# Performance work log

Hardware: AMD Instinct MI355X
Metric: run time of the kernel (lower is better)

Reference implementation:

```python
import math
import jax, jax.numpy as jnp
import numpy as np

D_MODEL = 1024
HID = 128
H, NB = 16, 16


def setup_inputs() -> dict:
    key = jax.random.key(0)
    ks = jax.random.split(key, 8)
    B, L = 4, 4096
    theta_path = jax.random.normal(ks[0], (B, L, H, NB), dtype=jnp.float32)
    content_emb = jax.random.normal(ks[1], (B, L, D_MODEL), dtype=jnp.float32)
    # measure_head params (PyTorch Linear default init: U(-1/sqrt(fan_in), 1/sqrt(fan_in)))
    s1 = 1.0 / math.sqrt(D_MODEL)
    s2 = 1.0 / math.sqrt(HID)
    W1 = jax.random.uniform(ks[2], (D_MODEL, HID), minval=-s1, maxval=s1, dtype=jnp.float32)
    b1 = jax.random.uniform(ks[3], (HID,), minval=-s1, maxval=s1, dtype=jnp.float32)
    W2 = jax.random.uniform(ks[4], (HID, H * NB), minval=-s2, maxval=s2, dtype=jnp.float32)
    b2 = jax.random.uniform(ks[5], (H * NB,), minval=-s2, maxval=s2, dtype=jnp.float32)
    log_Pi = jnp.zeros((H, NB), dtype=jnp.float32)
    log_R = jnp.zeros((H, NB), dtype=jnp.float32)
    return {"theta_path": theta_path, "content_emb": content_emb, "W1": W1, "b1": b1,
            "W2": W2, "b2": b2, "log_Pi": log_Pi, "log_R": log_R}


def _affine_scan(alpha, u):
    # d_t = alpha_t * d_{t-1} + u_t, d_0 = u_0 (zero initial state), scan over axis=1 (L)
    def combine(left, right):
        a_l, u_l = left
        a_r, u_r = right
        return a_l * a_r, a_r * u_l + u_r
    _, d = jax.lax.associative_scan(combine, (alpha, u), axis=1)
    return d


def reference(theta_path, content_emb, W1, b1, W2, b2, log_Pi, log_R):
    B, L, _, _ = theta_path.shape
    h = jax.nn.gelu(content_emb @ W1 + b1, approximate=False)  # [B,L,128], exact GELU as torch
    z = jnp.pi * jnp.tanh((h @ W2 + b2).reshape(B, L, H, NB))
    diff = z - theta_path
    nu = jnp.arctan2(jnp.sin(diff), jnp.cos(diff))  # wrapped angle residual
    Pi = jnp.exp(log_Pi)[None, None]  # [1,1,H,NB]
    R = jnp.exp(log_R)[None, None]
    K = Pi / jnp.maximum(Pi + R, 1e-08)
    Kf = jnp.broadcast_to(K, (B, L, H, NB))
    alpha = 1.0 - Kf
    u = Kf * nu
    d = _affine_scan(alpha, u)
    return (theta_path + d,
            jnp.broadcast_to(Pi, (B, L, H, NB)),
            Kf,
            jnp.broadcast_to(R, (B, L, H, NB)))
```

## Files before the change

### kernel.cpp

```cpp
#include <hip/hip_runtime.h>
#include <math.h>

#define MTOT  16384
#define DM    1024
#define HIDN  128
#define HNB   256
#define NBAT  4
#define CLK   32
#define NBLK  512
#define CPB   128

typedef _Float16 v8h __attribute__((ext_vector_type(8)));
typedef float    v4f __attribute__((ext_vector_type(4)));
#define MFMA16(a,b,c) __builtin_amdgcn_mfma_f32_16x16x32_f16((a),(b),(c),0,0,0)

#define W1TILE  16384
#define W2BASE  524288
#define W2TILE  32768
#define BLOB_BYTES 655360

#define RAWOFF 0
#define AHOFF  16384
#define ALOFF  20480
#define W1OFF  24576
#define HHOFF  40960
#define HLOFF  49664
#define ZOFF   0
#define SMEMSZ 73728

#define VMCNT_(N) asm volatile("s_waitcnt vmcnt(" #N ")" ::: "memory")
#define VMCNT(N) VMCNT_(N)
#define BARRIER() do { asm volatile("s_waitcnt lgkmcnt(0)" ::: "memory"); \
                       __builtin_amdgcn_s_barrier(); } while (0)

typedef const __attribute__((address_space(1))) void* gas1_t;
typedef __attribute__((address_space(3))) void* las3_t;

__device__ __forceinline__ void gld16(const void* g, void* l) {
    __builtin_amdgcn_global_load_lds((gas1_t)g, (las3_t)l, 16, 0, 0);
}

__global__ __launch_bounds__(256) void k_prep(
    const float* __restrict__ W1,
    const float* __restrict__ W2,
    char* __restrict__ blobs)
{
    __shared__ float lds[32][260];
    const int t = threadIdx.x, blk = blockIdx.x;
    if (blk < 32) {
        const int k0 = blk * 32;
        #pragma unroll
        for (int i = 0; i < 4; ++i) {
            int j = t + i * 256;
            int k = j >> 5, n4 = (j & 31) << 2;
            *(float4*)&lds[k][n4] = *(const float4*)&W1[(size_t)(k0 + k) * HIDN + n4];
        }
        __syncthreads();
        const int n = t >> 1, kh = t & 1;
        #pragma unroll
        for (int si = 0; si < 2; ++si) {
            const int s = 2 * kh + si;
            union { _Float16 h[8]; int4 v; } H, L;
            #pragma unroll
            for (int e = 0; e < 8; ++e) {
                float v = lds[s * 8 + e][n];
                _Float16 hh = (_Float16)v;
                H.h[e] = hh;
                L.h[e] = (_Float16)((v - (float)hh) * 4096.f);
            }
            char* d = blobs + blk * W1TILE + n * 64 + ((s ^ (n & 3)) << 4);
            *(int4*)d = H.v;
            *(int4*)(d + 8192) = L.v;
        }
    } else {
        const int ks = blk - 32, k0 = ks * 32;
        #pragma unroll
        for (int i = 0; i < 8; ++i) {
            int j = t + i * 256;
            int k = j >> 6, n4 = (j & 63) << 2;
            *(float4*)&lds[k][n4] = *(const float4*)&W2[(size_t)(k0 + k) * HNB + n4];
        }
        __syncthreads();
        const int n = t;
        #pragma unroll
        for (int s = 0; s < 4; ++s) {
            union { _Float16 h[8]; int4 v; } H, L;
            #pragma unroll
            for (int e = 0; e < 8; ++e) {
                float v = lds[s * 8 + e][n];
                _Float16 hh = (_Float16)v;
                H.h[e] = hh;
                L.h[e] = (_Float16)((v - (float)hh) * 4096.f);
            }
            char* d = blobs + W2BASE + ks * W2TILE + n * 64 + ((s ^ (n & 3)) << 4);
            *(int4*)d = H.v;
            *(int4*)(d + 16384) = L.v;
        }
    }
}

__global__ __launch_bounds__(512, 4) void k_mega(
    const float* __restrict__ A,
    const float* __restrict__ theta,
    const float* __restrict__ b1, const float* __restrict__ b2,
    const float* __restrict__ logPi, const float* __restrict__ logR,
    const char* __restrict__ blobs,
    float* __restrict__ out0, float* __restrict__ out2,
    float* fill1, float* fill3,
    float* carry, int cstride)
{
    __shared__ __attribute__((aligned(16))) char smem[SMEMSZ];

    const int tid  = threadIdx.x;
    const int blk  = blockIdx.x;
    const int m0   = blk * CLK;
    const int lane = tid & 63;
    const int wid  = tid >> 6;
    const int ln15 = lane & 15;
    const int q    = lane >> 4;
    const int np   = wid & 3;
    const int mh   = wid >> 2;

    const int rrow = (wid & 3) * 8 + (lane >> 3);
    const float* aStage = A + (size_t)(m0 + rrow) * DM + (lane & 7) * 4;
    const int rawDst = rrow * 128 + (lane & 7) * 16;

    const int crow = (wid & 3) * 8 + (lane >> 3);
    const int cvtRd = crow * 128 + (lane & 7) * 16;
    const int cs = (lane & 7) >> 1, chalf = (lane & 7) & 1;
    const int cvtWr = crow * 64 + ((cs ^ ((crow >> 1) & 3)) << 4) + chalf * 8;

    const int wq = wid & 3;
    const char* wSrcB = blobs + wq * 4096 + lane * 16;
    const int   wDstB = wq * 4096 + lane * 16;

    const int arow = 16 * mh + ln15;
    const int aby  = arow * 64 + ((q ^ ((arow >> 1) & 3)) << 4);
    const int col0 = 32 * np + ln15;
    const int col1 = col0 + 16;
    const int wo0  = col0 * 64 + ((q ^ (col0 & 3)) << 4);
    const int wo1  = col1 * 64 + ((q ^ (col1 & 3)) << 4);

    v4f acc1[2], acc2[2];
    acc1[0] = acc1[1] = (v4f){0.f, 0.f, 0.f, 0.f};
    acc2[0] = acc2[1] = (v4f){0.f, 0.f, 0.f, 0.f};

#define CVT(J) do { \
    const char* rb_ = smem + ((J) % 4) * 4096 + cvtRd; \
    v4f rv_ = *(const v4f*)rb_; \
    union { _Float16 h[4]; int2 i; } H_, L_; \
    _Pragma("unroll") \
    for (int e_ = 0; e_ < 4; ++e_) { \
        _Float16 t_ = (_Float16)rv_[e_]; \
        H_.h[e_] = t_; \
        L_.h[e_] = (_Float16)((rv_[e_] - (float)t_) * 4096.f); \
    } \
    *(int2*)(smem + AHOFF + ((J) & 1) * 2048 + cvtWr) = H_.i; \
    *(int2*)(smem + ALOFF + ((J) & 1) * 2048 + cvtWr) = L_.i; \
} while (0)

#define STEP(KT, RVM, WVM, DO_RAW, DO_W, DO_CVT) do { \
    if (wid < 4) { \
        if (DO_RAW) gld16(aStage + (size_t)((KT) + 4) * 32, \
                          smem + ((KT) % 4) * 4096 + rawDst); \
    } else if (DO_W) { \
        const char* ws_ = wSrcB + (size_t)((KT) + 2) * W1TILE; \
        char* wd_ = smem + W1OFF + (((KT) + 2) % 3) * W1TILE + wDstB; \
        gld16(ws_, wd_);                 gld16(ws_ + 1024, wd_ + 1024); \
        gld16(ws_ + 2048, wd_ + 2048);   gld16(ws_ + 3072, wd_ + 3072); \
    } \
    { \
        const char* abH = smem + AHOFF + ((KT) & 1) * 2048; \
        const char* abL = smem + ALOFF + ((KT) & 1) * 2048; \
        const char* wbB = smem + W1OFF + ((KT) % 3) * W1TILE; \
        v8h ah_  = *(const v8h*)(abH + aby); \
        v8h al_  = *(const v8h*)(abL + aby); \
        v8h wh0_ = *(const v8h*)(wbB + wo0); \
        v8h wl0_ = *(const v8h*)(wbB + 8192 + wo0); \
        v8h wh1_ = *(const v8h*)(wbB + wo1); \
        v8h wl1_ = *(const v8h*)(wbB + 8192 + wo1); \
        acc1[0] = MFMA16(ah_, wh0_, acc1[0]); \
        acc2[0] = MFMA16(ah_, wl0_, acc2[0]); \
        acc2[0] = MFMA16(al_, wh0_, acc2[0]); \
        acc1[1] = MFMA16(ah_, wh1_, acc1[1]); \
        acc2[1] = MFMA16(ah_, wl1_, acc2[1]); \
        acc2[1] = MFMA16(al_, wh1_, acc2[1]); \
    } \
    if (wid < 4) { VMCNT(RVM); if (DO_CVT) { CVT((KT) + 1); } } \
    else         { VMCNT(WVM); } \
    BARRIER(); \
} while (0)

    if (wid < 4) {
        gld16(aStage,      smem + 0 * 4096 + rawDst);
        gld16(aStage + 32, smem + 1 * 4096 + rawDst);
        gld16(aStage + 64, smem + 2 * 4096 + rawDst);
        gld16(aStage + 96, smem + 3 * 4096 + rawDst);
        VMCNT(3);
        CVT(0);
    } else {
        #pragma unroll
        for (int t = 0; t < 3; ++t) {
            const char* ws_ = wSrcB + (size_t)t * W1TILE;
            char* wd_ = smem + W1OFF + t * W1TILE + wDstB;
            gld16(ws_, wd_);               gld16(ws_ + 1024, wd_ + 1024);
            gld16(ws_ + 2048, wd_ + 2048); gld16(ws_ + 3072, wd_ + 3072);
        }
        VMCNT(8);
    }
    BARRIER();

    STEP(0,3,4,1,1,1);  STEP(1,3,4,1,1,1);  STEP(2,3,4,1,1,1);  STEP(3,3,4,1,1,1);
    STEP(4,3,4,1,1,1);  STEP(5,3,4,1,1,1);  STEP(6,3,4,1,1,1);  STEP(7,3,4,1,1,1);
    STEP(8,3,4,1,1,1);  STEP(9,3,4,1,1,1);  STEP(10,3,4,1,1,1); STEP(11,3,4,1,1,1);
    STEP(12,3,4,1,1,1); STEP(13,3,4,1,1,1); STEP(14,3,4,1,1,1); STEP(15,3,4,1,1,1);
    STEP(16,3,4,1,1,1); STEP(17,3,4,1,1,1); STEP(18,3,4,1,1,1); STEP(19,3,4,1,1,1);
    STEP(20,3,4,1,1,1); STEP(21,3,4,1,1,1); STEP(22,3,4,1,1,1); STEP(23,3,4,1,1,1);
    STEP(24,3,4,1,1,1); STEP(25,3,4,1,1,1); STEP(26,3,4,1,1,1); STEP(27,3,4,1,1,1);
    STEP(28,2,4,0,1,1); STEP(29,1,4,0,1,1); STEP(30,0,0,0,0,1); STEP(31,0,0,0,0,0);

    const float inv = 1.f / 4096.f;
    #pragma unroll
    for (int ni = 0; ni < 2; ++ni) {
        const int col = 32 * np + 16 * ni + ln15;
        const float bv = b1[col];
        #pragma unroll
        for (int r = 0; r < 4; ++r) {
            const int row = 16 * mh + 4 * q + r;
            float y = acc1[ni][r] + acc2[ni][r] * inv + bv;
            float h = 0.5f * y * (1.f + erff(y * 0.70710678118654752f));
            _Float16 hh = (_Float16)h;
            _Float16 hl = (_Float16)((h - (float)hh) * 4096.f);
            const int byte_ = row * 272 + ((((col >> 3) ^ ((row >> 1) & 3))) << 4)
                            + (col & 7) * 2;
            *(_Float16*)(smem + HHOFF + byte_) = hh;
            *(_Float16*)(smem + HLOFF + byte_) = hl;
        }
    }
    BARRIER();

    v4f c1[4], c2[4];
    #pragma unroll
    for (int i = 0; i < 4; ++i) {
        c1[i] = (v4f){0.f, 0.f, 0.f, 0.f};
        c2[i] = (v4f){0.f, 0.f, 0.f, 0.f};
    }
    const int hrow = 16 * mh + ln15;
    #pragma unroll
    for (int ks = 0; ks < 4; ++ks) {
        const int hby = hrow * 272 + ((4 * ks + (q ^ ((hrow >> 1) & 3))) << 4);
        v8h hh = *(const v8h*)(smem + HHOFF + hby);
        v8h hl = *(const v8h*)(smem + HLOFF + hby);
        v8h w2h[4], w2l[4];
        #pragma unroll
        for (int ni = 0; ni < 4; ++ni) {
            const int c2i = 64 * np + 16 * ni + ln15;
            const char* wp = blobs + W2BASE + (size_t)ks * W2TILE
                           + c2i * 64 + ((q ^ (c2i & 3)) << 4);
            w2h[ni] = *(const v8h*)(wp);
            w2l[ni] = *(const v8h*)(wp + 16384);
        }
        #pragma unroll
        for (int ni = 0; ni < 4; ++ni) {
            c1[ni] = MFMA16(hh, w2h[ni], c1[ni]);
            c2[ni] = MFMA16(hh, w2l[ni], c2[ni]);
            c2[ni] = MFMA16(hl, w2h[ni], c2[ni]);
        }
    }

    #pragma unroll
    for (int ni = 0; ni < 4; ++ni) {
        const int col = 64 * np + 16 * ni + ln15;
        const float bv = b2[col];
        #pragma unroll
        for (int r = 0; r < 4; ++r) {
            const int row = 16 * mh + 4 * q + r;
            float y2 = c1[ni][r] + c2[ni][r] * inv + bv;
            *(float*)(smem + ZOFF + row * 1040 + col * 4) =
                3.14159265358979323846f * tanhf(y2);
        }
    }
    BARRIER();

    if (tid < 256) {
        const int c = tid;
        const float Pi = expf(logPi[c]);
        const float Rr = expf(logR[c]);
        const float Kc = Pi / fmaxf(Pi + Rr, 1e-8f);
        const float alpha = 1.f - Kc;
        float d = 0.f;
        float tv[2][16];
        #pragma unroll
        for (int i = 0; i < 16; ++i)
            tv[0][i] = theta[(size_t)(m0 + i) * HNB + c];
        #pragma unroll
        for (int g = 0; g < 2; ++g) {
            if (g < 1) {
                #pragma unroll
                for (int i = 0; i < 16; ++i)
                    tv[1][i] = theta[(size_t)(m0 + 16 + i) * HNB + c];
            }
            float sv[16];
            #pragma unroll
            for (int i = 0; i < 16; ++i) {
                float z = *(const float*)(smem + ZOFF + (g * 16 + i) * 1040 + c * 4);
                float diff = z - tv[g][i];
                float kq = rintf(diff * 0.15915494309189533577f);
                float nu = (float)((double)diff - (double)kq * 6.283185307179586476925286766559);
                d = fmaf(alpha, d, Kc * nu);
                sv[i] = tv[g][i] + d;
            }
            #pragma unroll
            for (int i = 0; i < 16; ++i)
                out0[(size_t)(m0 + g * 16 + i) * HNB + c] = sv[i];
        }
        carry[(size_t)blk * cstride + c] = d;
    } else {
        const int c = tid - 256;
        const float Pi = expf(logPi[c]);
        const float Rr = expf(logR[c]);
        const float Kc = Pi / fmaxf(Pi + Rr, 1e-8f);
        if (fill1) {
            #pragma unroll 4
            for (int i = 0; i < CLK; ++i) {
                size_t idx = (size_t)(m0 + i) * HNB + c;
                out2[idx]  = Kc;
                fill1[idx] = Pi;
                fill3[idx] = Rr;
            }
        } else {
            #pragma unroll 4
            for (int i = 0; i < CLK; ++i)
                out2[(size_t)(m0 + i) * HNB + c] = Kc;
        }
    }
#undef STEP
#undef CVT
}

__global__ __launch_bounds__(256) void k_cscan(
    const float* __restrict__ logPi, const float* __restrict__ logR,
    float* carry, int cstride)
{
    const int c = threadIdx.x, b = blockIdx.x;
    const float Pi = expf(logPi[c]);
    const float Rr = expf(logR[c]);
    const float alpha = 1.f - Pi / fmaxf(Pi + Rr, 1e-8f);
    float A32 = alpha;
    #pragma unroll
    for (int i = 0; i < 5; ++i) A32 *= A32;
    float D = 0.f;
    for (int s0 = 0; s0 < CPB; s0 += 16) {
        float a[16];
        #pragma unroll
        for (int j = 0; j < 16; ++j)
            a[j] = carry[(size_t)(b * CPB + s0 + j) * cstride + c];
        #pragma unroll
        for (int j = 0; j < 16; ++j) {
            carry[(size_t)(b * CPB + s0 + j) * cstride + c] = D;
            D = fmaf(A32, D, a[j]);
        }
    }
}

__global__ __launch_bounds__(256) void k_apply(
    const float* __restrict__ logPi, const float* __restrict__ logR,
    float* __restrict__ out0, float* out1, float* out3,
    const float* carry, int cstride, int do_fills)
{
    const int blk = blockIdx.x;
    const int c = threadIdx.x;
    const float Pi = expf(logPi[c]);
    const float Rr = expf(logR[c]);
    const float Kc = Pi / fmaxf(Pi + Rr, 1e-8f);
    const float alpha = 1.f - Kc;
    float D = carry[(size_t)blk * cstride + c];
    float w = alpha * D;
    const size_t base = (size_t)blk * (CLK * HNB) + c;
    if (do_fills) {
        #pragma unroll 4
        for (int i = 0; i < CLK; ++i) {
            size_t idx = base + (size_t)i * HNB;
            out0[idx] += w;
            out1[idx] = Pi;
            out3[idx] = Rr;
            w *= alpha;
        }
    } else {
        #pragma unroll 4
        for (int i = 0; i < CLK; ++i) {
            size_t idx = base + (size_t)i * HNB;
            out0[idx] += w;
            w *= alpha;
        }
    }
}

extern "C" void kernel_launch(void* const* d_in, const int* in_sizes, int n_in,
                              void* d_out, int out_size, void* d_ws, size_t ws_size,
                              hipStream_t stream) {
    const float* theta   = (const float*)d_in[0];
    const float* content = (const float*)d_in[1];
    const float* W1      = (const float*)d_in[2];
    const float* b1      = (const float*)d_in[3];
    const float* W2      = (const float*)d_in[4];
    const float* b2      = (const float*)d_in[5];
    const float* logPi   = (const float*)d_in[6];
    const float* logR    = (const float*)d_in[7];

    float* out  = (float*)d_out;
    float* out0 = out;
    float* out1 = out + (size_t)MTOT * HNB;
    float* out2 = out + (size_t)2 * MTOT * HNB;
    float* out3 = out + (size_t)3 * MTOT * HNB;

    const size_t carry_bytes = (size_t)NBLK * 256 * 4;
    const size_t need = carry_bytes + BLOB_BYTES;
    float* carry; int cstride, do_fills; char* blobs;
    float *f1, *f3;
    if (ws_size >= need) {
        carry   = (float*)d_ws;
        cstride = 256;
        blobs   = (char*)d_ws + carry_bytes;
        f1 = out1; f3 = out3; do_fills = 0;
    } else {
        carry   = out3;
        cstride = CLK * HNB;
        blobs   = (char*)out1;
        f1 = nullptr; f3 = nullptr; do_fills = 1;
    }

    hipLaunchKernelGGL(k_prep, dim3(36), dim3(256), 0, stream, W1, W2, blobs);
    hipLaunchKernelGGL(k_mega, dim3(NBLK), dim3(512), 0, stream,
                       content, theta, b1, b2, logPi, logR, blobs,
                       out0, out2, f1, f3, carry, cstride);
    hipLaunchKernelGGL(k_cscan, dim3(NBAT), dim3(256), 0, stream,
                       logPi, logR, carry, cstride);
    hipLaunchKernelGGL(k_apply, dim3(NBLK), dim3(256), 0, stream,
                       logPi, logR, out0, out1, out3, carry, cstride, do_fills);
}
```

Measured before the change: 62.00 us.

## Store weights in MFMA fragment order and convert A in registers

Repacks the W1 and W2 half-precision split blobs into per-lane MFMA fragment order, so each lane loads one contiguous 16-byte chunk and the XOR swizzle is no longer needed. The A tile is loaded raw into LDS already in fragment order, and each wave now does the fp32 to hi/lo fp16 split in registers just before its MFMAs. This drops the separate CVT stage, its double-buffered converted-A LDS region, and the extra LDS write/read round trip. LDS usage drops to 64KB and the A prefetch depth goes from 4 tiles to 3, which may shorten latency hiding while improving occupancy headroom.

```diff
diff --git a/kernel.cpp b/kernel.cpp
--- a/kernel.cpp
+++ b/kernel.cpp
@@ -20,13 +20,11 @@
 #define BLOB_BYTES 655360
 
 #define RAWOFF 0
-#define AHOFF  16384
-#define ALOFF  20480
-#define W1OFF  24576
-#define HHOFF  40960
-#define HLOFF  49664
-#define ZOFF   0
-#define SMEMSZ 73728
+#define W1OFF  16384
+#define HHOFF  0
+#define HLOFF  8192
+#define ZOFF   16384
+#define SMEMSZ 65536
 
 #define VMCNT_(N) asm volatile("s_waitcnt vmcnt(" #N ")" ::: "memory")
 #define VMCNT(N) VMCNT_(N)
@@ -56,19 +54,20 @@
             *(float4*)&lds[k][n4] = *(const float4*)&W1[(size_t)(k0 + k) * HIDN + n4];
         }
         __syncthreads();
-        const int n = t >> 1, kh = t & 1;
-        #pragma unroll
-        for (int si = 0; si < 2; ++si) {
-            const int s = 2 * kh + si;
+        const int fl = t & 63, np = t >> 6;
+        const int kb = (fl >> 4) * 8;
+        #pragma unroll
+        for (int fi = 0; fi < 2; ++fi) {
+            const int col = 32 * np + 16 * fi + (fl & 15);
             union { _Float16 h[8]; int4 v; } H, L;
             #pragma unroll
             for (int e = 0; e < 8; ++e) {
-                float v = lds[s * 8 + e][n];
+                float v = lds[kb + e][col];
                 _Float16 hh = (_Float16)v;
                 H.h[e] = hh;
                 L.h[e] = (_Float16)((v - (float)hh) * 4096.f);
             }
-            char* d = blobs + blk * W1TILE + n * 64 + ((s ^ (n & 3)) << 4);
+            char* d = blobs + blk * W1TILE + np * 2048 + fi * 1024 + fl * 16;
             *(int4*)d = H.v;
             *(int4*)(d + 8192) = L.v;
         }
@@ -81,18 +80,21 @@
             *(float4*)&lds[k][n4] = *(const float4*)&W2[(size_t)(k0 + k) * HNB + n4];
         }
         __syncthreads();
-        const int n = t;
-        #pragma unroll
-        for (int s = 0; s < 4; ++s) {
+        const int fl = t & 63, cg0 = t >> 6;
+        const int kb = (fl >> 4) * 8;
+        #pragma unroll
+        for (int i = 0; i < 4; ++i) {
+            const int cg = cg0 * 4 + i;
+            const int col = cg * 16 + (fl & 15);
             union { _Float16 h[8]; int4 v; } H, L;
             #pragma unroll
             for (int e = 0; e < 8; ++e) {
-                float v = lds[s * 8 + e][n];
+                float v = lds[kb + e][col];
                 _Float16 hh = (_Float16)v;
                 H.h[e] = hh;
                 L.h[e] = (_Float16)((v - (float)hh) * 4096.f);
             }
-            char* d = blobs + W2BASE + ks * W2TILE + n * 64 + ((s ^ (n & 3)) << 4);
+            char* d = blobs + W2BASE + ks * W2TILE + cg * 1024 + fl * 16;
             *(int4*)d = H.v;
             *(int4*)(d + 16384) = L.v;
         }
@@ -121,118 +123,99 @@
     const int np   = wid & 3;
     const int mh   = wid >> 2;
 
-    const int rrow = (wid & 3) * 8 + (lane >> 3);
-    const float* aStage = A + (size_t)(m0 + rrow) * DM + (lane & 7) * 4;
-    const int rawDst = rrow * 128 + (lane & 7) * 16;
-
-    const int crow = (wid & 3) * 8 + (lane >> 3);
-    const int cvtRd = crow * 128 + (lane & 7) * 16;
-    const int cs = (lane & 7) >> 1, chalf = (lane & 7) & 1;
-    const int cvtWr = crow * 64 + ((cs ^ ((crow >> 1) & 3)) << 4) + chalf * 8;
+    const int mh_s = wid >> 1, half_s = wid & 1;
+    const float* aSrc = A + (size_t)(m0 + 16 * mh_s + ln15) * DM + q * 8 + half_s * 4;
+    const int rawDst = wid * 1024 + lane * 16;
 
     const int wq = wid & 3;
-    const char* wSrcB = blobs + wq * 4096 + lane * 16;
-    const int   wDstB = wq * 4096 + lane * 16;
-
-    const int arow = 16 * mh + ln15;
-    const int aby  = arow * 64 + ((q ^ ((arow >> 1) & 3)) << 4);
-    const int col0 = 32 * np + ln15;
-    const int col1 = col0 + 16;
-    const int wo0  = col0 * 64 + ((q ^ (col0 & 3)) << 4);
-    const int wo1  = col1 * 64 + ((q ^ (col1 & 3)) << 4);
+    const char* wSrc = blobs + wq * 2048 + (size_t)lane * 16;
+    const int   wDst = wq * 2048 + lane * 16;
 
     v4f acc1[2], acc2[2];
     acc1[0] = acc1[1] = (v4f){0.f, 0.f, 0.f, 0.f};
     acc2[0] = acc2[1] = (v4f){0.f, 0.f, 0.f, 0.f};
 
-#define CVT(J) do { \
-    const char* rb_ = smem + ((J) % 4) * 4096 + cvtRd; \
-    v4f rv_ = *(const v4f*)rb_; \
-    union { _Float16 h[4]; int2 i; } H_, L_; \
-    _Pragma("unroll") \
-    for (int e_ = 0; e_ < 4; ++e_) { \
-        _Float16 t_ = (_Float16)rv_[e_]; \
-        H_.h[e_] = t_; \
-        L_.h[e_] = (_Float16)((rv_[e_] - (float)t_) * 4096.f); \
-    } \
-    *(int2*)(smem + AHOFF + ((J) & 1) * 2048 + cvtWr) = H_.i; \
-    *(int2*)(smem + ALOFF + ((J) & 1) * 2048 + cvtWr) = L_.i; \
-} while (0)
-
-#define STEP(KT, RVM, WVM, DO_RAW, DO_W, DO_CVT) do { \
+#define STEP(KT, AV, WV, DO_RAW, DO_W) do { \
     if (wid < 4) { \
-        if (DO_RAW) gld16(aStage + (size_t)((KT) + 4) * 32, \
-                          smem + ((KT) % 4) * 4096 + rawDst); \
+        if (DO_RAW) gld16(aSrc + (size_t)((KT) + 3) * 32, \
+                          smem + RAWOFF + (((KT) + 3) & 3) * 4096 + rawDst); \
     } else if (DO_W) { \
-        const char* ws_ = wSrcB + (size_t)((KT) + 2) * W1TILE; \
-        char* wd_ = smem + W1OFF + (((KT) + 2) % 3) * W1TILE + wDstB; \
-        gld16(ws_, wd_);                 gld16(ws_ + 1024, wd_ + 1024); \
-        gld16(ws_ + 2048, wd_ + 2048);   gld16(ws_ + 3072, wd_ + 3072); \
+        const char* ws_ = wSrc + (size_t)((KT) + 2) * W1TILE; \
+        char* wd_ = smem + W1OFF + (((KT) + 2) % 3) * 16384 + wDst; \
+        gld16(ws_, wd_);             gld16(ws_ + 1024, wd_ + 1024); \
+        gld16(ws_ + 8192, wd_ + 8192); gld16(ws_ + 9216, wd_ + 9216); \
     } \
     { \
-        const char* abH = smem + AHOFF + ((KT) & 1) * 2048; \
-        const char* abL = smem + ALOFF + ((KT) & 1) * 2048; \
-        const char* wbB = smem + W1OFF + ((KT) % 3) * W1TILE; \
-        v8h ah_  = *(const v8h*)(abH + aby); \
-        v8h al_  = *(const v8h*)(abL + aby); \
-        v8h wh0_ = *(const v8h*)(wbB + wo0); \
-        v8h wl0_ = *(const v8h*)(wbB + 8192 + wo0); \
-        v8h wh1_ = *(const v8h*)(wbB + wo1); \
-        v8h wl1_ = *(const v8h*)(wbB + 8192 + wo1); \
-        acc1[0] = MFMA16(ah_, wh0_, acc1[0]); \
-        acc2[0] = MFMA16(ah_, wl0_, acc2[0]); \
-        acc2[0] = MFMA16(al_, wh0_, acc2[0]); \
-        acc1[1] = MFMA16(ah_, wh1_, acc1[1]); \
-        acc2[1] = MFMA16(ah_, wl1_, acc2[1]); \
-        acc2[1] = MFMA16(al_, wh1_, acc2[1]); \
+        const char* rawb = smem + RAWOFF + ((KT) & 3) * 4096 + mh * 2048 + lane * 16; \
+        v4f lo = *(const v4f*)rawb; \
+        v4f hi = *(const v4f*)(rawb + 1024); \
+        const char* wbB = smem + W1OFF + ((KT) % 3) * 16384 + np * 2048 + lane * 16; \
+        v8h wh0 = *(const v8h*)(wbB); \
+        v8h wh1 = *(const v8h*)(wbB + 1024); \
+        v8h wl0 = *(const v8h*)(wbB + 8192); \
+        v8h wl1 = *(const v8h*)(wbB + 9216); \
+        v8h ah, al; \
+        _Pragma("unroll") \
+        for (int e_ = 0; e_ < 4; ++e_) { \
+            _Float16 t0_ = (_Float16)lo[e_]; \
+            ah[e_] = t0_; \
+            al[e_] = (_Float16)((lo[e_] - (float)t0_) * 4096.f); \
+            _Float16 t1_ = (_Float16)hi[e_]; \
+            ah[e_ + 4] = t1_; \
+            al[e_ + 4] = (_Float16)((hi[e_] - (float)t1_) * 4096.f); \
+        } \
+        acc1[0] = MFMA16(ah, wh0, acc1[0]); \
+        acc2[0] = MFMA16(ah, wl0, acc2[0]); \
+        acc2[0] = MFMA16(al, wh0, acc2[0]); \
+        acc1[1] = MFMA16(ah, wh1, acc1[1]); \
+        acc2[1] = MFMA16(ah, wl1, acc2[1]); \
+        acc2[1] = MFMA16(al, wh1, acc2[1]); \
     } \
-    if (wid < 4) { VMCNT(RVM); if (DO_CVT) { CVT((KT) + 1); } } \
-    else         { VMCNT(WVM); } \
+    if (wid < 4) { VMCNT(AV); } else { VMCNT(WV); } \
     BARRIER(); \
 } while (0)
 
     if (wid < 4) {
-        gld16(aStage,      smem + 0 * 4096 + rawDst);
-        gld16(aStage + 32, smem + 1 * 4096 + rawDst);
-        gld16(aStage + 64, smem + 2 * 4096 + rawDst);
-        gld16(aStage + 96, smem + 3 * 4096 + rawDst);
-        VMCNT(3);
-        CVT(0);
+        gld16(aSrc,      smem + RAWOFF + 0 * 4096 + rawDst);
+        gld16(aSrc + 32, smem + RAWOFF + 1 * 4096 + rawDst);
+        gld16(aSrc + 64, smem + RAWOFF + 2 * 4096 + rawDst);
+        VMCNT(2);
     } else {
         #pragma unroll
-        for (int t = 0; t < 3; ++t) {
-            const char* ws_ = wSrcB + (size_t)t * W1TILE;
-            char* wd_ = smem + W1OFF + t * W1TILE + wDstB;
+        for (int t2 = 0; t2 < 2; ++t2) {
+            const char* ws_ = wSrc + (size_t)t2 * W1TILE;
+            char* wd_ = smem + W1OFF + t2 * 16384 + wDst;
             gld16(ws_, wd_);               gld16(ws_ + 1024, wd_ + 1024);
-            gld16(ws_ + 2048, wd_ + 2048); gld16(ws_ + 3072, wd_ + 3072);
-        }
-        VMCNT(8);
+            gld16(ws_ + 8192, wd_ + 8192); gld16(ws_ + 9216, wd_ + 9216);
+        }
+        VMCNT(4);
     }
     BARRIER();
 
-    STEP(0,3,4,1,1,1);  STEP(1,3,4,1,1,1);  STEP(2,3,4,1,1,1);  STEP(3,3,4,1,1,1);
-    STEP(4,3,4,1,1,1);  STEP(5,3,4,1,1,1);  STEP(6,3,4,1,1,1);  STEP(7,3,4,1,1,1);
-    STEP(8,3,4,1,1,1);  STEP(9,3,4,1,1,1);  STEP(10,3,4,1,1,1); STEP(11,3,4,1,1,1);
-    STEP(12,3,4,1,1,1); STEP(13,3,4,1,1,1); STEP(14,3,4,1,1,1); STEP(15,3,4,1,1,1);
-    STEP(16,3,4,1,1,1); STEP(17,3,4,1,1,1); STEP(18,3,4,1,1,1); STEP(19,3,4,1,1,1);
-    STEP(20,3,4,1,1,1); STEP(21,3,4,1,1,1); STEP(22,3,4,1,1,1); STEP(23,3,4,1,1,1);
-    STEP(24,3,4,1,1,1); STEP(25,3,4,1,1,1); STEP(26,3,4,1,1,1); STEP(27,3,4,1,1,1);
-    STEP(28,2,4,0,1,1); STEP(29,1,4,0,1,1); STEP(30,0,0,0,0,1); STEP(31,0,0,0,0,0);
+    STEP(0,2,4,1,1);  STEP(1,2,4,1,1);  STEP(2,2,4,1,1);  STEP(3,2,4,1,1);
+    STEP(4,2,4,1,1);  STEP(5,2,4,1,1);  STEP(6,2,4,1,1);  STEP(7,2,4,1,1);
+    STEP(8,2,4,1,1);  STEP(9,2,4,1,1);  STEP(10,2,4,1,1); STEP(11,2,4,1,1);
+    STEP(12,2,4,1,1); STEP(13,2,4,1,1); STEP(14,2,4,1,1); STEP(15,2,4,1,1);
+    STEP(16,2,4,1,1); STEP(17,2,4,1,1); STEP(18,2,4,1,1); STEP(19,2,4,1,1);
+    STEP(20,2,4,1,1); STEP(21,2,4,1,1); STEP(22,2,4,1,1); STEP(23,2,4,1,1);
+    STEP(24,2,4,1,1); STEP(25,2,4,1,1); STEP(26,2,4,1,1); STEP(27,2,4,1,1);
+    STEP(28,2,4,1,1); STEP(29,1,4,0,1); STEP(30,0,0,0,0); STEP(31,0,0,0,0);
 
     const float inv = 1.f / 4096.f;
     #pragma unroll
     for (int ni = 0; ni < 2; ++ni) {
-        const int col = 32 * np + 16 * ni + ln15;
-        const float bv = b1[col];
+        const int colH = 32 * np + 16 * ni + ln15;
+        const float bv = b1[colH];
+        const int qH = (colH >> 3) & 3;
+        const int eH = colH & 7;
         #pragma unroll
         for (int r = 0; r < 4; ++r) {
-            const int row = 16 * mh + 4 * q + r;
             float y = acc1[ni][r] + acc2[ni][r] * inv + bv;
             float h = 0.5f * y * (1.f + erff(y * 0.70710678118654752f));
             _Float16 hh = (_Float16)h;
             _Float16 hl = (_Float16)((h - (float)hh) * 4096.f);
-            const int byte_ = row * 272 + ((((col >> 3) ^ ((row >> 1) & 3))) << 4)
-                            + (col & 7) * 2;
+            const int fl = (4 * q + r) + 16 * qH;
+            const int byte_ = mh * 4096 + np * 1024 + fl * 16 + eH * 2;
             *(_Float16*)(smem + HHOFF + byte_) = hh;
             *(_Float16*)(smem + HLOFF + byte_) = hl;
         }
@@ -245,26 +228,19 @@
         c1[i] = (v4f){0.f, 0.f, 0.f, 0.f};
         c2[i] = (v4f){0.f, 0.f, 0.f, 0.f};
     }
-    const int hrow = 16 * mh + ln15;
     #pragma unroll
     for (int ks = 0; ks < 4; ++ks) {
-        const int hby = hrow * 272 + ((4 * ks + (q ^ ((hrow >> 1) & 3))) << 4);
-        v8h hh = *(const v8h*)(smem + HHOFF + hby);
-        v8h hl = *(const v8h*)(smem + HLOFF + hby);
-        v8h w2h[4], w2l[4];
+        v8h hh = *(const v8h*)(smem + HHOFF + mh * 4096 + ks * 1024 + lane * 16);
+        v8h hl = *(const v8h*)(smem + HLOFF + mh * 4096 + ks * 1024 + lane * 16);
         #pragma unroll
         for (int ni = 0; ni < 4; ++ni) {
-            const int c2i = 64 * np + 16 * ni + ln15;
             const char* wp = blobs + W2BASE + (size_t)ks * W2TILE
-                           + c2i * 64 + ((q ^ (c2i & 3)) << 4);
-            w2h[ni] = *(const v8h*)(wp);
-            w2l[ni] = *(const v8h*)(wp + 16384);
-        }
-        #pragma unroll
-        for (int ni = 0; ni < 4; ++ni) {
-            c1[ni] = MFMA16(hh, w2h[ni], c1[ni]);
-            c2[ni] = MFMA16(hh, w2l[ni], c2[ni]);
-            c2[ni] = MFMA16(hl, w2h[ni], c2[ni]);
+                           + (4 * np + ni) * 1024 + (size_t)lane * 16;
+            v8h w2h = *(const v8h*)wp;
+            v8h w2l = *(const v8h*)(wp + 16384);
+            c1[ni] = MFMA16(hh, w2h, c1[ni]);
+            c2[ni] = MFMA16(hh, w2l, c2[ni]);
+            c2[ni] = MFMA16(hl, w2h, c2[ni]);
         }
     }
 
@@ -335,7 +311,6 @@
         }
     }
 #undef STEP
-#undef CVT
 }
 
 __global__ __launch_bounds__(256) void k_cscan(
```

After: 62.61 us. Within noise of the previous version (+1.0%).
